# Kernel tuning notes

Hardware: AMD Instinct MI355X
Metric: run time of the kernel (lower is better)

## Reference

```python
import jax, jax.numpy as jnp
import numpy as np

MAX_CH = 21
LAT_DIM = 64
D_EMBED = 1024
N_HEADS = 16
D_HEAD = D_EMBED // N_HEADS  # 64
L = MAX_CH * LAT_DIM         # 1344 latents
B, T = 4, 1024


def setup_inputs() -> dict:
    key = jax.random.key(0)
    k1, k2, k3, k4, k5, k6 = jax.random.split(key, 6)
    x = jax.random.normal(k1, (B, T, D_EMBED), dtype=jnp.float32)
    # boolean channel mask [b, L, T]
    ch_mask = jax.random.randint(k2, (B, L, T), 0, 2) > 0
    # learned latent queries [L, H*d] (xavier-uniform-ish init)
    lim_q = float(np.sqrt(6.0 / (L + N_HEADS * D_HEAD)))
    latent_q = jax.random.uniform(k3, (L, N_HEADS * D_HEAD), minval=-lim_q, maxval=lim_q, dtype=jnp.float32)
    # Linear weights (torch layout: [out, in]) and biases
    lim_w = float(np.sqrt(1.0 / D_EMBED))
    w_k_w = jax.random.uniform(k4, (N_HEADS * D_HEAD, D_EMBED), minval=-lim_w, maxval=lim_w, dtype=jnp.float32)
    w_k_b = jnp.zeros((N_HEADS * D_HEAD,), dtype=jnp.float32)
    w_v_w = jax.random.uniform(k5, (N_HEADS * D_HEAD, D_EMBED), minval=-lim_w, maxval=lim_w, dtype=jnp.float32)
    w_v_b = jax.random.uniform(k6, (N_HEADS * D_HEAD,), minval=-lim_w, maxval=lim_w, dtype=jnp.float32)
    return {"x": x, "ch_mask": ch_mask, "latent_q": latent_q,
            "w_k_w": w_k_w, "w_k_b": w_k_b, "w_v_w": w_v_w, "w_v_b": w_v_b}


def reference(x, ch_mask, latent_q, w_k_w, w_k_b, w_v_w, w_v_b):
    b, t, d = x.shape
    H, dh = N_HEADS, D_HEAD
    l = latent_q.shape[0]
    # faithful to torch .view(-1, H, L, d): raw row-major reinterpretation
    lq = latent_q.reshape(1, H, l, dh)                    # [1,H,L,dh]
    k = (x @ w_k_w.T + w_k_b).reshape(b, t, H, dh).transpose(0, 2, 3, 1)  # [b,H,dh,T]
    v = (x @ w_v_w.T + w_v_b).reshape(b, t, H, dh).transpose(0, 2, 1, 3)  # [b,H,T,dh]
    scale = jnp.float32(H) ** -0.5  # note: n_heads**-0.5, as in source
    scores = jnp.einsum('ohld,bhdt->bhlt', lq, k) * scale  # [b,H,L,T]
    mask = ch_mask[:, None, :, :]                           # [b,1,L,T] broadcast over heads
    scores = jnp.where(mask, scores, jnp.float32(-1e9))
    w = jax.nn.softmax(scores, axis=-1)
    w = jnp.where(mask, w, jnp.float32(0.0))
    out = jnp.einsum('bhlt,bhtd->bhld', w, v)               # [b,H,L,dh]
    return out.transpose(0, 2, 1, 3).reshape(b, l, H * dh)  # [b,L,H*dh]
```

## Files before the change

### kernel.cpp

```cpp
#include <hip/hip_runtime.h>
#include <hip/hip_bf16.h>

#define B_SZ 4
#define T_SZ 1024
#define NH 16
#define L_SZ 1344
#define LT_COUNT 21

typedef __attribute__((ext_vector_type(8))) short short8;
typedef __attribute__((ext_vector_type(4))) short short4v;
typedef __attribute__((ext_vector_type(4))) float floatx4;

typedef __attribute__((address_space(1))) const void gvoid;
typedef __attribute__((address_space(3))) void svoid;
#define GLD16(gp, lp) \
  __builtin_amdgcn_global_load_lds((gvoid*)(gp), (svoid*)(lp), 16, 0, 0)

static __device__ inline short bf16bits(float f) {
  return __builtin_bit_cast(short, __float2bfloat16(f));
}
static __device__ inline short4v cvt4(float4 v) {
  short4v r;
  r.x = bf16bits(v.x); r.y = bf16bits(v.y);
  r.z = bf16bits(v.z); r.w = bf16bits(v.w);
  return r;
}

static __device__ inline unsigned pack_bf16_2(float a, float b) {
  unsigned ua = __builtin_bit_cast(unsigned, a) + 0x8000u;
  unsigned ub = __builtin_bit_cast(unsigned, b) + 0x8000u;
  return __builtin_amdgcn_perm(ub, ua, 0x07060302u);
}
static __device__ inline uint2 pack_bf16_4(float4 v) {
  return make_uint2(pack_bf16_2(v.x, v.y), pack_bf16_2(v.z, v.w));
}


__global__ __launch_bounds__(256) void mask_detect(
    const unsigned char* __restrict__ m, int* __restrict__ flag) {
  __shared__ int any_off4, any_at4;
  if (threadIdx.x == 0) { any_off4 = 0; any_at4 = 0; }
  __syncthreads();
  int a1 = 0, a2 = 0;
  for (int i = threadIdx.x; i < 4096; i += 256) {
    unsigned char v = m[i];
    if (v) {
      if ((i & 3) != 0) a1 = 1;
      if ((i & 7) == 4) a2 = 1;
    }
  }
  if (a1) atomicOr(&any_off4, 1);
  if (a2) atomicOr(&any_at4, 1);
  __syncthreads();
  if (threadIdx.x == 0) *flag = any_off4 ? 1 : (any_at4 ? 0 : 2);
}

__global__ __launch_bounds__(256) void maskbits_kernel(
    const void* __restrict__ mask, const int* __restrict__ flag,
    unsigned int* __restrict__ bits) {
  int idx = blockIdx.x * 256 + threadIdx.x;
  int f = *flag;
  bool v;
  if (f == 1)      v = ((const signed char*)mask)[idx] != 0;
  else if (f == 2) v = ((const long long*)mask)[idx] != 0;
  else             v = ((const int*)mask)[idx] != 0;
  unsigned long long bal = __ballot(v);
  int lane = threadIdx.x & 63;
  if ((lane & 31) == 0) {
    unsigned int w = (lane & 32) ? (unsigned int)(bal >> 32) : (unsigned int)bal;
    bits[idx >> 5] = w;
  }
}

__global__ __launch_bounds__(256) void cvt_bf16(
    const float4* __restrict__ src, uint2* __restrict__ dst) {
  size_t i = (size_t)blockIdx.x * 256 + threadIdx.x;
  dst[i] = pack_bf16_4(src[i]);
}

static __device__ __forceinline__ void epi_k(const floatx4 acc[4][4],
    int bxt, int byd, int wm, int wn, int c15, int kq,
    const float* __restrict__ bk, __hip_bfloat16* __restrict__ k_buf) {
  #pragma unroll
  for (int ni = 0; ni < 4; ++ni) {
    int gr = bxt * 128 + wn * 64 + ni * 16 + c15;
    int b = gr >> 10, tc = (gr >> 6) & 15;
    #pragma unroll
    for (int mi = 0; mi < 4; ++mi) {
      int d0 = byd * 128 + wm * 64 + mi * 16 + kq * 4;
      int h = d0 >> 6, hd = d0 & 63;
      int half = hd >> 5, q4 = (hd >> 3) & 3, jlo = hd & 7;
      int bh = b * 16 + h;
      float4 b4 = *(const float4*)(bk + d0);
      float4 v4 = {acc[mi][ni][0] + b4.x, acc[mi][ni][1] + b4.y,
                   acc[mi][ni][2] + b4.z, acc[mi][ni][3] + b4.w};
      *(uint2*)(k_buf + ((size_t)((bh * 16 + tc) * 8 + ni * 2 + half)) * 512 +
                (q4 * 16 + c15) * 8 + jlo) = pack_bf16_4(v4);
    }
  }
}

static __device__ __forceinline__ void epi_v(const floatx4 acc[4][4],
    int bxd, int byt, int wm, int wn, int c15, int kq,
    const float* __restrict__ bv, __hip_bfloat16* __restrict__ v_buf) {
  #pragma unroll
  for (int ni = 0; ni < 4; ++ni) {
    int d = bxd * 128 + wn * 64 + ni * 16 + c15;
    int h = d >> 6;
    float bias = bv[d];
    #pragma unroll
    for (int mi = 0; mi < 4; ++mi) {
      int gr = byt * 128 + wm * 64 + mi * 16 + kq * 4;
      int b = gr >> 10, tc = (gr >> 6) & 15;
      int tl = gr & 63;
      int half = tl >> 5, q4 = (tl >> 3) & 3, jlo = tl & 7;
      int bh = b * 16 + h;
      float4 v4 = {acc[mi][ni][0] + bias, acc[mi][ni][1] + bias,
                   acc[mi][ni][2] + bias, acc[mi][ni][3] + bias};
      *(uint2*)(v_buf + ((size_t)((bh * 16 + tc) * 8 + ni * 2 + half)) * 512 +
                (q4 * 16 + c15) * 8 + jlo) = pack_bf16_4(v4);
    }
  }
}

static __device__ __forceinline__ void gemm_core(
    const __hip_bfloat16* __restrict__ A, const __hip_bfloat16* __restrict__ B,
    __hip_bfloat16* ldsA, __hip_bfloat16* ldsB,
    int TA, int TB, int tid, floatx4 (&acc)[4][4]) {
  const int lane = tid & 63, w = tid >> 6;
  const int wm = w & 1, wn = w >> 1;
  const int c15 = lane & 15, kq = lane >> 4;
  for (int kk = 0; kk < 1024; kk += 32) {
    #pragma unroll
    for (int j = 0; j < 2; ++j) {
      int c = w * 128 + j * 64 + lane;
      int row = c >> 2;
      int gkc = (c & 3) ^ (row & 3);
      GLD16(A + (size_t)(TA * 128 + row) * 1024 + kk + gkc * 8,
            ldsA + (w * 128 + j * 64) * 8);
      GLD16(B + (size_t)(TB * 128 + row) * 1024 + kk + gkc * 8,
            ldsB + (w * 128 + j * 64) * 8);
    }
    __syncthreads();
    short8 af[4], bf[4];
    #pragma unroll
    for (int mi = 0; mi < 4; ++mi) {
      int row = wm * 64 + mi * 16 + c15;
      af[mi] = *(const short8*)(ldsA + row * 32 + ((kq ^ (row & 3)) * 8));
    }
    #pragma unroll
    for (int ni = 0; ni < 4; ++ni) {
      int row = wn * 64 + ni * 16 + c15;
      bf[ni] = *(const short8*)(ldsB + row * 32 + ((kq ^ (row & 3)) * 8));
    }
    #pragma unroll
    for (int mi = 0; mi < 4; ++mi)
      #pragma unroll
      for (int ni = 0; ni < 4; ++ni)
        acc[mi][ni] = __builtin_amdgcn_mfma_f32_16x16x32_bf16(
            af[mi], bf[ni], acc[mi][ni], 0, 0, 0);
    __syncthreads();
  }
}

__global__ __launch_bounds__(256) void gemm_kv_bf16(
    const __hip_bfloat16* __restrict__ xb,
    const __hip_bfloat16* __restrict__ wkb, const __hip_bfloat16* __restrict__ wvb,
    const float* __restrict__ bk, const float* __restrict__ bv,
    __hip_bfloat16* __restrict__ k_buf, __hip_bfloat16* __restrict__ v_buf) {
  __shared__ __align__(16) __hip_bfloat16 ldsA[128 * 32];
  __shared__ __align__(16) __hip_bfloat16 ldsB[128 * 32];
  const int tid = threadIdx.x;
  const int lane = tid & 63, w = tid >> 6;
  const int wm = w & 1, wn = w >> 1;
  const int c15 = lane & 15, kq = lane >> 4;
  floatx4 acc[4][4];
  for (int i = 0; i < 4; ++i)
    for (int j = 0; j < 4; ++j) acc[i][j] = (floatx4){0.f, 0.f, 0.f, 0.f};

  if (blockIdx.z == 0) {
    gemm_core(wkb, xb, ldsA, ldsB, blockIdx.y, blockIdx.x, tid, acc);
    epi_k(acc, blockIdx.x, blockIdx.y, wm, wn, c15, kq, bk, k_buf);
  } else {
    gemm_core(xb, wvb, ldsA, ldsB, blockIdx.x, blockIdx.y, tid, acc);
    epi_v(acc, blockIdx.y, blockIdx.x, wm, wn, c15, kq, bv, v_buf);
  }
}

__global__ __launch_bounds__(64, 2) void attn_kernel(
    const float* __restrict__ latent_q,
    const __hip_bfloat16* __restrict__ k_buf,
    const __hip_bfloat16* __restrict__ v_buf,
    const unsigned int* __restrict__ mbits,
    float* __restrict__ out) {
  __shared__ __align__(16) __hip_bfloat16 pbuf[4][16 * 72];
  __shared__ uint2 mrows[64][17];

  const int lane = threadIdx.x & 63;
  int bid = blockIdx.x;
  int xcd = bid & 7, j = bid >> 3;
  int bh = xcd * 8 + j / LT_COUNT;
  int lt = j % LT_COUNT;
  int h = bh & 15, b = bh >> 4;
  const int q4 = lane >> 4, c15 = lane & 15;
  const int l0 = lt * 64;

  {
    const unsigned int* msrc = mbits + (size_t)(b * L_SZ + l0) * 32;
    #pragma unroll
    for (int p = 0; p < 8; ++p) {
      int i = p * 64 + lane;
      uint4 m4 = *(const uint4*)(msrc + i * 4);
      int row = i >> 3, c2 = (i & 7) * 2;
      mrows[row][c2]     = make_uint2(m4.x, m4.y);
      mrows[row][c2 + 1] = make_uint2(m4.z, m4.w);
    }
  }

  const float QS = 0.25f * 1.44269504089f;
  short8 qf[4][2];
  #pragma unroll
  for (int g = 0; g < 4; ++g) {
    const float* qp = latent_q + ((size_t)(h * L_SZ + l0 + g * 16 + c15)) * 64 + q4 * 8;
    float4 a0 = *(const float4*)(qp);
    float4 a1 = *(const float4*)(qp + 4);
    float4 a2 = *(const float4*)(qp + 32);
    float4 a3 = *(const float4*)(qp + 36);
    a0.x *= QS; a0.y *= QS; a0.z *= QS; a0.w *= QS;
    a1.x *= QS; a1.y *= QS; a1.z *= QS; a1.w *= QS;
    a2.x *= QS; a2.y *= QS; a2.z *= QS; a2.w *= QS;
    a3.x *= QS; a3.y *= QS; a3.z *= QS; a3.w *= QS;
    short4v t0 = cvt4(a0), t1 = cvt4(a1), t2 = cvt4(a2), t3 = cvt4(a3);
    qf[g][0] = (short8){t0.x, t0.y, t0.z, t0.w, t1.x, t1.y, t1.z, t1.w};
    qf[g][1] = (short8){t2.x, t2.y, t2.z, t2.w, t3.x, t3.y, t3.z, t3.w};
  }

  floatx4 l4[4];
  floatx4 o_acc[4][4];
  #pragma unroll
  for (int g = 0; g < 4; ++g) {
    l4[g] = (floatx4){0.f, 0.f, 0.f, 0.f};
    #pragma unroll
    for (int di = 0; di < 4; ++di) o_acc[g][di] = (floatx4){0.f, 0.f, 0.f, 0.f};
  }

  const __hip_bfloat16* kb = k_buf + (size_t)bh * 65536;
  const __hip_bfloat16* vb = v_buf + (size_t)bh * 65536;

  for (int tc = 0; tc < 16; ++tc) {
    short8 kf[2][4], vf[2][4];
    #pragma unroll
    for (int half = 0; half < 2; ++half)
      #pragma unroll
      for (int ni = 0; ni < 4; ++ni)
        kf[half][ni] = *(const short8*)(kb + (size_t)(tc * 8 + ni * 2 + half) * 512 + lane * 8);
    #pragma unroll
    for (int half = 0; half < 2; ++half)
      #pragma unroll
      for (int di = 0; di < 4; ++di)
        vf[half][di] = *(const short8*)(vb + (size_t)(tc * 8 + di * 2 + half) * 512 + lane * 8);

    #pragma unroll
    for (int g = 0; g < 4; ++g) {
      uint2 mw = mrows[g * 16 + c15][tc];
      floatx4 s[4];
      #pragma unroll
      for (int ni = 0; ni < 4; ++ni) s[ni] = (floatx4){0.f, 0.f, 0.f, 0.f};
      #pragma unroll
      for (int half = 0; half < 2; ++half)
        #pragma unroll
        for (int ni = 0; ni < 4; ++ni)
          s[ni] = __builtin_amdgcn_mfma_f32_16x16x32_bf16(kf[half][ni], qf[g][half], s[ni], 0, 0, 0);
      __hip_bfloat16* pw = pbuf[g];
      #pragma unroll
      for (int ni = 0; ni < 4; ++ni) {
        unsigned mword = (ni >= 2) ? mw.y : mw.x;
        float4 p4;
        #pragma unroll
        for (int r = 0; r < 4; ++r) {
          float e = exp2f(s[ni][r]);
          int sh = (ni & 1) * 16 + q4 * 4 + r;
          ((float*)&p4)[r] = ((mword >> sh) & 1) ? e : 0.f;
        }
        l4[g][0] += p4.x; l4[g][1] += p4.y;
        l4[g][2] += p4.z; l4[g][3] += p4.w;
        *(uint2*)(pw + c15 * 72 + ni * 16 + q4 * 4) = pack_bf16_4(p4);
      }
    }

    #pragma unroll
    for (int g = 0; g < 4; ++g) {
      short8 pf0 = *(const short8*)(pbuf[g] + c15 * 72 + q4 * 8);
      short8 pf1 = *(const short8*)(pbuf[g] + c15 * 72 + 32 + q4 * 8);
      #pragma unroll
      for (int di = 0; di < 4; ++di)
        o_acc[g][di] = __builtin_amdgcn_mfma_f32_16x16x32_bf16(vf[0][di], pf0, o_acc[g][di], 0, 0, 0);
      #pragma unroll
      for (int di = 0; di < 4; ++di)
        o_acc[g][di] = __builtin_amdgcn_mfma_f32_16x16x32_bf16(vf[1][di], pf1, o_acc[g][di], 0, 0, 0);
    }
  }

  #pragma unroll
  for (int g = 0; g < 4; ++g) {
    float la = (l4[g][0] + l4[g][1]) + (l4[g][2] + l4[g][3]);
    la += __shfl_xor(la, 16, 64);
    la += __shfl_xor(la, 32, 64);
    float inv = (la > 0.f) ? 1.f / la : 0.f;
    float* ob = out + ((size_t)(b * L_SZ + l0 + g * 16 + c15)) * 1024 + h * 64;
    #pragma unroll
    for (int di = 0; di < 4; ++di) {
      float4 o4 = {o_acc[g][di][0] * inv, o_acc[g][di][1] * inv,
                   o_acc[g][di][2] * inv, o_acc[g][di][3] * inv};
      *(float4*)(ob + di * 16 + q4 * 4) = o4;
    }
  }
}

extern "C" void kernel_launch(void* const* d_in, const int* in_sizes, int n_in,
                              void* d_out, int out_size, void* d_ws, size_t ws_size,
                              hipStream_t stream) {
  const float* x      = (const float*)d_in[0];
  const void* ch_mask = d_in[1];
  const float* lq     = (const float*)d_in[2];
  const float* wk     = (const float*)d_in[3];
  const float* bk     = (const float*)d_in[4];
  const float* wv     = (const float*)d_in[5];
  const float* bv     = (const float*)d_in[6];
  float* out = (float*)d_out;

  char* ws = (char*)d_ws;
  unsigned int* mbits   = (unsigned int*)ws;
  int* flag             = (int*)(ws + 720896);
  __hip_bfloat16* k_buf = (__hip_bfloat16*)(ws + 786432);
  __hip_bfloat16* v_buf = (__hip_bfloat16*)(ws + 786432 + 8388608);

  __hip_bfloat16* xb  = (__hip_bfloat16*)d_out;
  __hip_bfloat16* wkb = xb + 4 * 1024 * 1024;
  __hip_bfloat16* wvb = wkb + 1024 * 1024;

  mask_detect<<<1, 256, 0, stream>>>((const unsigned char*)ch_mask, flag);
  maskbits_kernel<<<21504, 256, 0, stream>>>(ch_mask, flag, mbits);

  cvt_bf16<<<4096, 256, 0, stream>>>((const float4*)x, (uint2*)xb);
  cvt_bf16<<<1024, 256, 0, stream>>>((const float4*)wk, (uint2*)wkb);
  cvt_bf16<<<1024, 256, 0, stream>>>((const float4*)wv, (uint2*)wvb);
  gemm_kv_bf16<<<dim3(32, 8, 2), 256, 0, stream>>>(xb, wkb, wvb, bk, bv, k_buf, v_buf);

  attn_kernel<<<8 * 168, 64, 0, stream>>>(lq, k_buf, v_buf, mbits, out);
}
```

Baseline: 219.7 us.

## Split attention key dimension across four waves with LDS reduction

The attention kernel grows from one wave to four waves per block. Each wave handles a quarter of the T chunks for the same 64 latents, and the partial outputs and row sums are combined through shared memory before normalisation and the store. This gives four times as many waves in flight to hide K/V load and exp latency, which matters because 1344 single-wave blocks underfill the GPU. The cost is extra LDS for the reduction buffers, several block barriers in the epilogue, and tighter register limits from the new launch bounds.

```diff
diff --git a/kernel.cpp b/kernel.cpp
--- a/kernel.cpp
+++ b/kernel.cpp
@@ -187,7 +187,7 @@
   }
 }
 
-__global__ __launch_bounds__(64, 2) void attn_kernel(
+__global__ __launch_bounds__(256, 3) void attn_kernel(
     const float* __restrict__ latent_q,
     const __hip_bfloat16* __restrict__ k_buf,
     const __hip_bfloat16* __restrict__ v_buf,
@@ -195,8 +195,12 @@
     float* __restrict__ out) {
   __shared__ __align__(16) __hip_bfloat16 pbuf[4][16 * 72];
   __shared__ uint2 mrows[64][17];
-
-  const int lane = threadIdx.x & 63;
+  __shared__ float obuf[4][16][64];
+  __shared__ float lbuf[16][16];
+
+  const int tid = threadIdx.x;
+  const int lane = tid & 63;
+  const int w = tid >> 6;
   int bid = blockIdx.x;
   int xcd = bid & 7, j = bid >> 3;
   int bh = xcd * 8 + j / LT_COUNT;
@@ -208,14 +212,15 @@
   {
     const unsigned int* msrc = mbits + (size_t)(b * L_SZ + l0) * 32;
     #pragma unroll
-    for (int p = 0; p < 8; ++p) {
-      int i = p * 64 + lane;
+    for (int p = 0; p < 2; ++p) {
+      int i = p * 256 + tid;
       uint4 m4 = *(const uint4*)(msrc + i * 4);
       int row = i >> 3, c2 = (i & 7) * 2;
       mrows[row][c2]     = make_uint2(m4.x, m4.y);
       mrows[row][c2 + 1] = make_uint2(m4.z, m4.w);
     }
   }
+  __syncthreads();
 
   const float QS = 0.25f * 1.44269504089f;
   short8 qf[4][2];
@@ -247,7 +252,8 @@
   const __hip_bfloat16* kb = k_buf + (size_t)bh * 65536;
   const __hip_bfloat16* vb = v_buf + (size_t)bh * 65536;
 
-  for (int tc = 0; tc < 16; ++tc) {
+  for (int tci = 0; tci < 4; ++tci) {
+    const int tc = (w << 2) | tci;
     short8 kf[2][4], vf[2][4];
     #pragma unroll
     for (int half = 0; half < 2; ++half)
@@ -271,7 +277,7 @@
         #pragma unroll
         for (int ni = 0; ni < 4; ++ni)
           s[ni] = __builtin_amdgcn_mfma_f32_16x16x32_bf16(kf[half][ni], qf[g][half], s[ni], 0, 0, 0);
-      __hip_bfloat16* pw = pbuf[g];
+      __hip_bfloat16* pw = pbuf[w];
       #pragma unroll
       for (int ni = 0; ni < 4; ++ni) {
         unsigned mword = (ni >= 2) ? mw.y : mw.x;
@@ -286,12 +292,8 @@
         l4[g][2] += p4.z; l4[g][3] += p4.w;
         *(uint2*)(pw + c15 * 72 + ni * 16 + q4 * 4) = pack_bf16_4(p4);
       }
-    }
-
-    #pragma unroll
-    for (int g = 0; g < 4; ++g) {
-      short8 pf0 = *(const short8*)(pbuf[g] + c15 * 72 + q4 * 8);
-      short8 pf1 = *(const short8*)(pbuf[g] + c15 * 72 + 32 + q4 * 8);
+      short8 pf0 = *(const short8*)(pw + c15 * 72 + q4 * 8);
+      short8 pf1 = *(const short8*)(pw + c15 * 72 + 32 + q4 * 8);
       #pragma unroll
       for (int di = 0; di < 4; ++di)
         o_acc[g][di] = __builtin_amdgcn_mfma_f32_16x16x32_bf16(vf[0][di], pf0, o_acc[g][di], 0, 0, 0);
@@ -301,19 +303,39 @@
     }
   }
 
+  float la[4];
   #pragma unroll
   for (int g = 0; g < 4; ++g) {
-    float la = (l4[g][0] + l4[g][1]) + (l4[g][2] + l4[g][3]);
-    la += __shfl_xor(la, 16, 64);
-    la += __shfl_xor(la, 32, 64);
-    float inv = (la > 0.f) ? 1.f / la : 0.f;
-    float* ob = out + ((size_t)(b * L_SZ + l0 + g * 16 + c15)) * 1024 + h * 64;
-    #pragma unroll
-    for (int di = 0; di < 4; ++di) {
-      float4 o4 = {o_acc[g][di][0] * inv, o_acc[g][di][1] * inv,
-                   o_acc[g][di][2] * inv, o_acc[g][di][3] * inv};
-      *(float4*)(ob + di * 16 + q4 * 4) = o4;
-    }
+    la[g] = (l4[g][0] + l4[g][1]) + (l4[g][2] + l4[g][3]);
+    la[g] += __shfl_xor(la[g], 16, 64);
+    la[g] += __shfl_xor(la[g], 32, 64);
+  }
+  if (q4 == 0) {
+    #pragma unroll
+    for (int g = 0; g < 4; ++g) lbuf[w * 4 + g][c15] = la[g];
+  }
+  #pragma unroll
+  for (int g = 0; g < 4; ++g) {
+    #pragma unroll
+    for (int di = 0; di < 4; ++di)
+      #pragma unroll
+      for (int r = 0; r < 4; ++r)
+        obuf[w][di * 4 + r][lane] = o_acc[g][di][r];
+    __syncthreads();
+    float ltot = lbuf[g][c15] + lbuf[4 + g][c15] +
+                 lbuf[8 + g][c15] + lbuf[12 + g][c15];
+    float inv = (ltot > 0.f) ? 1.f / ltot : 0.f;
+    float4 o4;
+    #pragma unroll
+    for (int r = 0; r < 4; ++r) {
+      int k = w * 4 + r;
+      ((float*)&o4)[r] = (obuf[0][k][lane] + obuf[1][k][lane] +
+                          obuf[2][k][lane] + obuf[3][k][lane]) * inv;
+    }
+    float* ob = out + ((size_t)(b * L_SZ + l0 + g * 16 + c15)) * 1024 +
+                h * 64 + w * 16 + q4 * 4;
+    *(float4*)ob = o4;
+    if (g < 3) __syncthreads();
   }
 }
 
@@ -347,5 +369,5 @@
   cvt_bf16<<<1024, 256, 0, stream>>>((const float4*)wv, (uint2*)wvb);
   gemm_kv_bf16<<<dim3(32, 8, 2), 256, 0, stream>>>(xb, wkb, wvb, bk, bv, k_buf, v_buf);
 
-  attn_kernel<<<8 * 168, 64, 0, stream>>>(lq, k_buf, v_buf, mbits, out);
-}
+  attn_kernel<<<8 * 168, 256, 0, stream>>>(lq, k_buf, v_buf, mbits, out);
+}
```

Measured after the change: 258.3 us. 1.18x slower.

## Split attention block's four latent groups across four waves

Applied to the files above, without the earlier changes.

The attention kernel goes from one wave handling all four 16-row latent groups to a 256-thread block where each wave handles one group. The mask staging is shared across threads and followed by a barrier. The goal is to cut per-wave register pressure and serial work so more waves run concurrently and latency is hidden better. The trade-off is that each wave now loads the K/V fragments itself, so global/L2 traffic for K and V rises fourfold per block.

```diff
diff --git a/kernel.cpp b/kernel.cpp
--- a/kernel.cpp
+++ b/kernel.cpp
@@ -187,7 +187,7 @@
   }
 }
 
-__global__ __launch_bounds__(64, 2) void attn_kernel(
+__global__ __launch_bounds__(256, 3) void attn_kernel(
     const float* __restrict__ latent_q,
     const __hip_bfloat16* __restrict__ k_buf,
     const __hip_bfloat16* __restrict__ v_buf,
@@ -196,7 +196,9 @@
   __shared__ __align__(16) __hip_bfloat16 pbuf[4][16 * 72];
   __shared__ uint2 mrows[64][17];
 
-  const int lane = threadIdx.x & 63;
+  const int tid = threadIdx.x;
+  const int lane = tid & 63;
+  const int w = tid >> 6;
   int bid = blockIdx.x;
   int xcd = bid & 7, j = bid >> 3;
   int bh = xcd * 8 + j / LT_COUNT;
@@ -208,20 +210,20 @@
   {
     const unsigned int* msrc = mbits + (size_t)(b * L_SZ + l0) * 32;
     #pragma unroll
-    for (int p = 0; p < 8; ++p) {
-      int i = p * 64 + lane;
+    for (int p = 0; p < 2; ++p) {
+      int i = p * 256 + tid;
       uint4 m4 = *(const uint4*)(msrc + i * 4);
       int row = i >> 3, c2 = (i & 7) * 2;
       mrows[row][c2]     = make_uint2(m4.x, m4.y);
       mrows[row][c2 + 1] = make_uint2(m4.z, m4.w);
     }
   }
+  __syncthreads();
 
   const float QS = 0.25f * 1.44269504089f;
-  short8 qf[4][2];
-  #pragma unroll
-  for (int g = 0; g < 4; ++g) {
-    const float* qp = latent_q + ((size_t)(h * L_SZ + l0 + g * 16 + c15)) * 64 + q4 * 8;
+  short8 qf[2];
+  {
+    const float* qp = latent_q + ((size_t)(h * L_SZ + l0 + w * 16 + c15)) * 64 + q4 * 8;
     float4 a0 = *(const float4*)(qp);
     float4 a1 = *(const float4*)(qp + 4);
     float4 a2 = *(const float4*)(qp + 32);
@@ -231,21 +233,18 @@
     a2.x *= QS; a2.y *= QS; a2.z *= QS; a2.w *= QS;
     a3.x *= QS; a3.y *= QS; a3.z *= QS; a3.w *= QS;
     short4v t0 = cvt4(a0), t1 = cvt4(a1), t2 = cvt4(a2), t3 = cvt4(a3);
-    qf[g][0] = (short8){t0.x, t0.y, t0.z, t0.w, t1.x, t1.y, t1.z, t1.w};
-    qf[g][1] = (short8){t2.x, t2.y, t2.z, t2.w, t3.x, t3.y, t3.z, t3.w};
-  }
-
-  floatx4 l4[4];
-  floatx4 o_acc[4][4];
+    qf[0] = (short8){t0.x, t0.y, t0.z, t0.w, t1.x, t1.y, t1.z, t1.w};
+    qf[1] = (short8){t2.x, t2.y, t2.z, t2.w, t3.x, t3.y, t3.z, t3.w};
+  }
+
+  floatx4 l4 = (floatx4){0.f, 0.f, 0.f, 0.f};
+  floatx4 o_acc[4];
   #pragma unroll
-  for (int g = 0; g < 4; ++g) {
-    l4[g] = (floatx4){0.f, 0.f, 0.f, 0.f};
-    #pragma unroll
-    for (int di = 0; di < 4; ++di) o_acc[g][di] = (floatx4){0.f, 0.f, 0.f, 0.f};
-  }
+  for (int di = 0; di < 4; ++di) o_acc[di] = (floatx4){0.f, 0.f, 0.f, 0.f};
 
   const __hip_bfloat16* kb = k_buf + (size_t)bh * 65536;
   const __hip_bfloat16* vb = v_buf + (size_t)bh * 65536;
+  __hip_bfloat16* pw = pbuf[w];
 
   for (int tc = 0; tc < 16; ++tc) {
     short8 kf[2][4], vf[2][4];
@@ -260,60 +259,50 @@
       for (int di = 0; di < 4; ++di)
         vf[half][di] = *(const short8*)(vb + (size_t)(tc * 8 + di * 2 + half) * 512 + lane * 8);
 
-    #pragma unroll
-    for (int g = 0; g < 4; ++g) {
-      uint2 mw = mrows[g * 16 + c15][tc];
-      floatx4 s[4];
-      #pragma unroll
-      for (int ni = 0; ni < 4; ++ni) s[ni] = (floatx4){0.f, 0.f, 0.f, 0.f};
-      #pragma unroll
-      for (int half = 0; half < 2; ++half)
-        #pragma unroll
-        for (int ni = 0; ni < 4; ++ni)
-          s[ni] = __builtin_amdgcn_mfma_f32_16x16x32_bf16(kf[half][ni], qf[g][half], s[ni], 0, 0, 0);
-      __hip_bfloat16* pw = pbuf[g];
-      #pragma unroll
-      for (int ni = 0; ni < 4; ++ni) {
-        unsigned mword = (ni >= 2) ? mw.y : mw.x;
-        float4 p4;
-        #pragma unroll
-        for (int r = 0; r < 4; ++r) {
-          float e = exp2f(s[ni][r]);
-          int sh = (ni & 1) * 16 + q4 * 4 + r;
-          ((float*)&p4)[r] = ((mword >> sh) & 1) ? e : 0.f;
-        }
-        l4[g][0] += p4.x; l4[g][1] += p4.y;
-        l4[g][2] += p4.z; l4[g][3] += p4.w;
-        *(uint2*)(pw + c15 * 72 + ni * 16 + q4 * 4) = pack_bf16_4(p4);
+    uint2 mw = mrows[w * 16 + c15][tc];
+    floatx4 s[4];
+    #pragma unroll
+    for (int ni = 0; ni < 4; ++ni) s[ni] = (floatx4){0.f, 0.f, 0.f, 0.f};
+    #pragma unroll
+    for (int half = 0; half < 2; ++half)
+      #pragma unroll
+      for (int ni = 0; ni < 4; ++ni)
+        s[ni] = __builtin_amdgcn_mfma_f32_16x16x32_bf16(kf[half][ni], qf[half], s[ni], 0, 0, 0);
+    #pragma unroll
+    for (int ni = 0; ni < 4; ++ni) {
+      unsigned mword = (ni >= 2) ? mw.y : mw.x;
+      float4 p4;
+      #pragma unroll
+      for (int r = 0; r < 4; ++r) {
+        float e = exp2f(s[ni][r]);
+        int sh = (ni & 1) * 16 + q4 * 4 + r;
+        ((float*)&p4)[r] = ((mword >> sh) & 1) ? e : 0.f;
       }
-    }
-
-    #pragma unroll
-    for (int g = 0; g < 4; ++g) {
-      short8 pf0 = *(const short8*)(pbuf[g] + c15 * 72 + q4 * 8);
-      short8 pf1 = *(const short8*)(pbuf[g] + c15 * 72 + 32 + q4 * 8);
-      #pragma unroll
-      for (int di = 0; di < 4; ++di)
-        o_acc[g][di] = __builtin_amdgcn_mfma_f32_16x16x32_bf16(vf[0][di], pf0, o_acc[g][di], 0, 0, 0);
-      #pragma unroll
-      for (int di = 0; di < 4; ++di)
-        o_acc[g][di] = __builtin_amdgcn_mfma_f32_16x16x32_bf16(vf[1][di], pf1, o_acc[g][di], 0, 0, 0);
-    }
-  }
-
+      l4[0] += p4.x; l4[1] += p4.y;
+      l4[2] += p4.z; l4[3] += p4.w;
+      *(uint2*)(pw + c15 * 72 + ni * 16 + q4 * 4) = pack_bf16_4(p4);
+    }
+
+    short8 pf0 = *(const short8*)(pw + c15 * 72 + q4 * 8);
+    short8 pf1 = *(const short8*)(pw + c15 * 72 + 32 + q4 * 8);
+    #pragma unroll
+    for (int di = 0; di < 4; ++di)
+      o_acc[di] = __builtin_amdgcn_mfma_f32_16x16x32_bf16(vf[0][di], pf0, o_acc[di], 0, 0, 0);
+    #pragma unroll
+    for (int di = 0; di < 4; ++di)
+      o_acc[di] = __builtin_amdgcn_mfma_f32_16x16x32_bf16(vf[1][di], pf1, o_acc[di], 0, 0, 0);
+  }
+
+  float la = (l4[0] + l4[1]) + (l4[2] + l4[3]);
+  la += __shfl_xor(la, 16, 64);
+  la += __shfl_xor(la, 32, 64);
+  float inv = (la > 0.f) ? 1.f / la : 0.f;
+  float* ob = out + ((size_t)(b * L_SZ + l0 + w * 16 + c15)) * 1024 + h * 64;
   #pragma unroll
-  for (int g = 0; g < 4; ++g) {
-    float la = (l4[g][0] + l4[g][1]) + (l4[g][2] + l4[g][3]);
-    la += __shfl_xor(la, 16, 64);
-    la += __shfl_xor(la, 32, 64);
-    float inv = (la > 0.f) ? 1.f / la : 0.f;
-    float* ob = out + ((size_t)(b * L_SZ + l0 + g * 16 + c15)) * 1024 + h * 64;
-    #pragma unroll
-    for (int di = 0; di < 4; ++di) {
-      float4 o4 = {o_acc[g][di][0] * inv, o_acc[g][di][1] * inv,
-                   o_acc[g][di][2] * inv, o_acc[g][di][3] * inv};
-      *(float4*)(ob + di * 16 + q4 * 4) = o4;
-    }
+  for (int di = 0; di < 4; ++di) {
+    float4 o4 = {o_acc[di][0] * inv, o_acc[di][1] * inv,
+                 o_acc[di][2] * inv, o_acc[di][3] * inv};
+    *(float4*)(ob + di * 16 + q4 * 4) = o4;
   }
 }
 
@@ -347,5 +336,5 @@
   cvt_bf16<<<1024, 256, 0, stream>>>((const float4*)wv, (uint2*)wvb);
   gemm_kv_bf16<<<dim3(32, 8, 2), 256, 0, stream>>>(xb, wkb, wvb, bk, bv, k_buf, v_buf);
 
-  attn_kernel<<<8 * 168, 64, 0, stream>>>(lq, k_buf, v_buf, mbits, out);
-}
+  attn_kernel<<<8 * 168, 256, 0, stream>>>(lq, k_buf, v_buf, mbits, out);
+}
```

Measured after the change: 207.7 us. -5.5%, faster.
